# Performance work log

Hardware: AMD Instinct MI355X
Metric: run time of the kernel (lower is better)

## Reference

```python
import jax, jax.numpy as jnp
import numpy as np

B, T, D_IN, D_H, N_H = 8, 1024, 512, 64, 8
PAD_TAIL = 128


def setup_inputs() -> dict:
    key = jax.random.key(0)
    ks = jax.random.split(key, 7)
    keys = jax.random.normal(ks[0], (B, T, D_IN), jnp.float32)
    queries = jax.random.normal(ks[1], (B, T, D_IN), jnp.float32)
    values = jax.random.normal(ks[2], (B, T, D_IN), jnp.float32)
    # truncated_normal(stddev=0.01) in the original; plain normal*0.01 is a faithful stand-in
    Wk = jax.random.normal(ks[3], (D_IN, D_H, N_H), jnp.float32) * 0.01
    Wq = jax.random.normal(ks[4], (D_IN, D_H, N_H), jnp.float32) * 0.01
    Wv = jax.random.normal(ks[5], (D_IN, D_H, N_H), jnp.float32) * 0.01
    key_seq = jax.random.randint(ks[6], (B, T), 0, 32000)
    key_seq = key_seq.at[:, -PAD_TAIL:].set(-1)  # -1 marks padding positions
    return {"keys": keys, "queries": queries, "values": values,
            "Wk": Wk, "Wq": Wq, "Wv": Wv, "key_seq": key_seq}


def reference(keys, queries, values, Wk, Wq, Wv, key_seq):
    # projections: (b, t, i) x (i, d, h) -> (b, t, d, h)
    Kh = jnp.einsum('bti,idh->btdh', keys, Wk)
    Qh = jnp.einsum('bti,idh->btdh', queries, Wq)
    Vh = jnp.einsum('bti,idh->btdh', values, Wv)

    # scores: i indexes keys, j indexes queries -> (b, Tk, Tq, h)
    scores = jnp.einsum('bidh,bjdh->bijh', Kh, Qh)

    dt = scores.dtype
    # padding mask over key positions (key_seq == -1 -> -1000)
    pad_mask = (-1000.0 * (1.0 - jnp.sign(key_seq + 1).astype(dt)))[:, :, None, None]
    # causal mask: disallow key index i > query index j (matrix_band_part(_, 0, -1) keeps i<=j)
    Tk, Tq = Kh.shape[1], Qh.shape[1]
    caus_mask = -1000.0 * jnp.tril(jnp.ones((Tk, Tq), dt), k=-1)
    mask = pad_mask + caus_mask[None, :, :, None]

    # NB: original adds mask BEFORE scaling, so the -1000 is also scaled. Keep that order.
    hidden_size = Kh.shape[2]
    scores = (scores + mask) / (hidden_size ** 0.5)

    # softmax over the key axis (axis=1)
    attn = jax.nn.softmax(scores, axis=1)

    # aggregate values: (b, i, j, h) x (b, i, d, h) -> (b, j, d, h)
    h_t = jnp.einsum('bijh,bidh->bjdh', attn, Vh)

    # tf.concat(tf.split(h_t, H, axis=-1), axis=2)[:, :, :, 0]
    # == per-head feature blocks laid out head-major along the feature axis
    b, j, d, nh = h_t.shape
    return h_t.transpose(0, 1, 3, 2).reshape(b, j, nh * d)
```

## Files before the change

kernel.cpp:

```cpp
#include <hip/hip_runtime.h>
#include <hip/hip_bf16.h>

#define B_SZ 8
#define T_SZ 1024
#define D_IN 512
#define D_H  64
#define N_H  8

typedef __hip_bfloat16 bf16;
using short8  = __attribute__((ext_vector_type(8))) short;
using short4v = __attribute__((ext_vector_type(4))) short;
using f32x4   = __attribute__((ext_vector_type(4))) float;

__device__ __forceinline__ unsigned short f2bf(float f) {
    union { __hip_bfloat16 b; unsigned short u; } c;
    c.b = __float2bfloat16(f);
    return c.u;
}

__device__ __forceinline__ void glds16(const unsigned short* g, unsigned short* l) {
    __builtin_amdgcn_global_load_lds(
        (const __attribute__((address_space(1))) unsigned int*)g,
        (__attribute__((address_space(3))) unsigned int*)l, 16, 0, 0);
}

__global__ __launch_bounds__(256) void wt_kernel(
    const float* __restrict__ Wk, const float* __restrict__ Wq,
    const float* __restrict__ Wv, unsigned short* __restrict__ Wt)
{
    const int mat = blockIdx.y;
    const float* W = (mat == 0) ? Wk : (mat == 1) ? Wq : Wv;
    int idx = blockIdx.x * 256 + threadIdx.x;
    float v = W[idx];
    int k = idx >> 9, c = idx & 511;
    int h = c & 7, d = c >> 3;
    int ks = (k & ~63) | ((k & 63) ^ ((d & 7) << 3));
    Wt[(((size_t)mat * 8 + h) * 64 + d) * 512 + ks] = f2bf(v);
}

__global__ __launch_bounds__(256, 3) void proj_kernel(
    const float* __restrict__ keys, const float* __restrict__ queries,
    const float* __restrict__ values,
    const unsigned short* __restrict__ Wt, unsigned short* __restrict__ KQVb)
{
    const int tid = threadIdx.x;
    const int m0  = blockIdx.x * 128;
    const int n0  = blockIdx.y * 128;
    const int mat = blockIdx.z;

    const float* X = (mat == 0) ? keys : (mat == 1) ? queries : values;
    const unsigned short* WT = Wt + (size_t)mat * (512 * 512);
    unsigned short* P = KQVb + (size_t)mat * ((size_t)B_SZ * N_H * T_SZ * D_H);

    __shared__ __align__(16) unsigned short Xst[128 * 64];
    __shared__ __align__(16) unsigned short Wst[2][128 * 64];

    const int wid = tid >> 6, lane = tid & 63;
    const int quad = lane >> 4, l15 = lane & 15;
    const int wr = (wid >> 1) * 64, wc = (wid & 1) * 64;

    const int ur = tid >> 3, uch = tid & 7;
    const int wrow  = wid * 32 + (lane >> 3);
    const int wcol8 = (lane & 7) * 8;

    f32x4 acc[4][4];
    #pragma unroll
    for (int i = 0; i < 4; ++i)
        #pragma unroll
        for (int n = 0; n < 4; ++n) acc[i][n] = (f32x4){0.f, 0.f, 0.f, 0.f};

    const float4* X4 = (const float4*)X;

    #pragma unroll
    for (int q = 0; q < 4; ++q)
        glds16(&WT[(size_t)(n0 + wrow + q * 8) * 512 + wcol8],
               &Wst[0][(wid * 4 + q) * 512]);
    float4 xr[4][2];
    #pragma unroll
    for (int q = 0; q < 4; ++q) {
        int r = ur + q * 32;
        xr[q][0] = X4[(size_t)(m0 + r) * 128 + uch * 2];
        xr[q][1] = X4[(size_t)(m0 + r) * 128 + uch * 2 + 1];
    }

    int wb = 0;
    for (int kc = 0; kc < 8; ++kc) {
        #pragma unroll
        for (int q = 0; q < 4; ++q) {
            int r = ur + q * 32;
            float4 a = xr[q][0], b = xr[q][1];
            short8 s8 = {(short)f2bf(a.x), (short)f2bf(a.y),
                         (short)f2bf(a.z), (short)f2bf(a.w),
                         (short)f2bf(b.x), (short)f2bf(b.y),
                         (short)f2bf(b.z), (short)f2bf(b.w)};
            *(short8*)&Xst[r * 64 + ((uch * 8) ^ ((r & 7) << 3))] = s8;
        }
        if (kc < 7) {
            const int k0n = (kc + 1) * 64;
            #pragma unroll
            for (int q = 0; q < 4; ++q)
                glds16(&WT[(size_t)(n0 + wrow + q * 8) * 512 + k0n + wcol8],
                       &Wst[wb ^ 1][(wid * 4 + q) * 512]);
            #pragma unroll
            for (int q = 0; q < 4; ++q) {
                int r = ur + q * 32;
                xr[q][0] = X4[(size_t)(m0 + r) * 128 + (k0n >> 2) + uch * 2];
                xr[q][1] = X4[(size_t)(m0 + r) * 128 + (k0n >> 2) + uch * 2 + 1];
            }
        }
        asm volatile("s_waitcnt lgkmcnt(0)" ::: "memory");
        __builtin_amdgcn_s_barrier();

        #pragma unroll
        for (int ic = 0; ic < 2; ++ic) {
            const int sc = ic * 32 + quad * 8;
            short8 af[4], bfr[4];
            #pragma unroll
            for (int mt = 0; mt < 4; ++mt) {
                int r = wr + mt * 16 + l15;
                af[mt] = *(const short8*)&Xst[r * 64 + (sc ^ ((r & 7) << 3))];
            }
            #pragma unroll
            for (int nt = 0; nt < 4; ++nt) {
                int r = wc + nt * 16 + l15;
                bfr[nt] = *(const short8*)&Wst[wb][r * 64 + (sc ^ ((r & 7) << 3))];
            }
            #pragma unroll
            for (int mt = 0; mt < 4; ++mt)
                #pragma unroll
                for (int nt = 0; nt < 4; ++nt)
                    acc[mt][nt] = __builtin_amdgcn_mfma_f32_16x16x32_bf16(
                        af[mt], bfr[nt], acc[mt][nt], 0, 0, 0);
        }

        asm volatile("s_waitcnt lgkmcnt(0)" ::: "memory");
        __builtin_amdgcn_s_barrier();
        wb ^= 1;
    }

    #pragma unroll
    for (int mt = 0; mt < 4; ++mt)
        #pragma unroll
        for (int r = 0; r < 4; ++r) {
            int mrow = m0 + wr + mt * 16 + quad * 4 + r;
            int bb = mrow >> 10, t = mrow & 1023;
            #pragma unroll
            for (int nt = 0; nt < 4; ++nt) {
                int c = n0 + wc + nt * 16 + l15;
                int h = c >> 6, d = c & 63;
                P[(((size_t)(bb * N_H + h)) * T_SZ + t) * D_H + d] =
                    f2bf(acc[mt][nt][r]);
            }
        }
}

#define SCALE  0.18033688f
#define MASKV -180.33688f

__global__ __launch_bounds__(512, 4) void attn_kernel(
    const unsigned short* __restrict__ Qb, const unsigned short* __restrict__ Kb,
    const unsigned short* __restrict__ Vb,
    const int* __restrict__ key_seq, float* __restrict__ out)
{
    const int tid  = threadIdx.x;
    const int bid  = blockIdx.x;
    const int pair = bid >> 6;
    const int b    = (bid >> 3) & 7;
    const int h    = bid & 7;
    const int wid  = tid >> 6, lane = tid & 63;
    const int quad = lane >> 4, l15 = lane & 15;

    __shared__ __align__(16) unsigned short Kst[2][64 * 72];
    __shared__ __align__(16) unsigned short VTst[2][64 * 72];
    __shared__ __align__(16) float spadf[2][64];
    __shared__ int tflags[16];

    const size_t bh = (size_t)(b * N_H + h) * T_SZ;

    const int strip_j0 = (wid < 4) ? (15 - pair) * 64 : pair * 64;
    const int j0w = strip_j0 + (wid & 3) * 16;
    const int jg  = j0w + l15;
    const int ntmax = 16 - pair;

    short8 qf0 = *(const short8*)&Qb[(bh + jg) * D_H + quad * 8];
    short8 qf1 = *(const short8*)&Qb[(bh + jg) * D_H + 32 + quad * 8];

    {
        int ka  = key_seq[b * T_SZ + wid * 64 + lane];
        int kb2 = key_seq[b * T_SZ + 512 + wid * 64 + lane];
        unsigned long long ba  = __ballot(ka  != -1);
        unsigned long long bb2 = __ballot(kb2 != -1);
        if (lane == 0) {
            tflags[wid]     = (ba  != 0ull ? 1 : 0) | (ba  != ~0ull ? 2 : 0);
            tflags[8 + wid] = (bb2 != 0ull ? 1 : 0) | (bb2 != ~0ull ? 2 : 0);
        }
    }

    const int sk_row = tid >> 3, sk_c = tid & 7;
    const int sv_i = lane, sv_ch = wid;
    const int sv_col = (sv_i & 3) | ((sv_i & 16) >> 2) | ((sv_i & 4) << 1)
                     | ((sv_i & 8) << 1) | (sv_i & 32);

    short8 kreg = *(const short8*)&Kb[(bh + sk_row) * D_H + sk_c * 8];
    short8 vreg = *(const short8*)&Vb[(bh + sv_i) * D_H + sv_ch * 8];
    int ksv = (tid < 64) ? key_seq[b * T_SZ + tid] : -1;

    __syncthreads();

    unsigned tmask = 1u, pmask = 0u;
    #pragma unroll
    for (int t = 0; t < 16; ++t) {
        int f = tflags[t];
        tmask |= (unsigned)(f & 1) << t;
        pmask |= (unsigned)((f >> 1) & 1) << t;
    }
    tmask &= (unsigned)((1ull << ntmax) - 1ull);
    tmask |= 1u;

    *(short8*)&Kst[0][sk_row * 72 + sk_c * 8] = kreg;
    #pragma unroll
    for (int e = 0; e < 8; ++e)
        VTst[0][(sv_ch * 8 + e) * 72 + sv_col] = (unsigned short)vreg[e];
    if (tid < 64) spadf[0][tid] = (ksv == -1) ? MASKV : 0.f;
    __syncthreads();

    float m = -1e30f, l = 0.f;
    f32x4 o0 = {0.f,0.f,0.f,0.f}, o1 = o0, o2 = o0, o3 = o0;

    unsigned rem = tmask & ~1u;
    int tcur = 0, nb = 0;
    for (;;) {
        int tnext = -1;
        if (rem) { tnext = __ffs((int)rem) - 1; rem &= rem - 1; }
        if (tnext >= 0) {
            const size_t r0 = bh + tnext * 64;
            kreg = *(const short8*)&Kb[(r0 + sk_row) * D_H + sk_c * 8];
            vreg = *(const short8*)&Vb[(r0 + sv_i) * D_H + sv_ch * 8];
            if (tid < 64) ksv = key_seq[b * T_SZ + tnext * 64 + tid];
        }

        const int i0 = tcur * 64;
        if (i0 <= j0w + 15) {
            const bool haspad = (pmask >> tcur) & 1u;
            const bool needC  = (i0 + 63 > j0w);
            float sv[16];
            #pragma unroll
            for (int it = 0; it < 4; ++it) {
                f32x4 s = {0.f,0.f,0.f,0.f};
                short8 a0 = *(const short8*)&Kst[nb][(it*16 + l15) * 72 + quad*8];
                s = __builtin_amdgcn_mfma_f32_16x16x32_bf16(a0, qf0, s, 0, 0, 0);
                short8 a1 = *(const short8*)&Kst[nb][(it*16 + l15) * 72 + 32 + quad*8];
                s = __builtin_amdgcn_mfma_f32_16x16x32_bf16(a1, qf1, s, 0, 0, 0);
                f32x4 sp = {0.f,0.f,0.f,0.f};
                if (haspad) sp = *(const f32x4*)&spadf[nb][it*16 + quad*4];
                #pragma unroll
                for (int r = 0; r < 4; ++r) {
                    float v = __builtin_fmaf(s[r], SCALE, sp[r]);
                    if (needC && (i0 + it*16 + quad*4 + r > jg)) v += MASKV;
                    sv[it*4 + r] = v;
                }
            }

            float mt = sv[0];
            #pragma unroll
            for (int k = 1; k < 16; ++k) mt = fmaxf(mt, sv[k]);
            mt = fmaxf(mt, __shfl_xor(mt, 16));
            mt = fmaxf(mt, __shfl_xor(mt, 32));
            const float mnew  = fmaxf(m, mt);
            const float alpha = exp2f(m - mnew);
            float p[16], ls = 0.f;
            #pragma unroll
            for (int k = 0; k < 16; ++k) {
                p[k] = exp2f(sv[k] - mnew);
                ls += p[k];
            }
            ls += __shfl_xor(ls, 16);
            ls += __shfl_xor(ls, 32);
            l = l * alpha + ls;
            m = mnew;
            o0 *= alpha; o1 *= alpha; o2 *= alpha; o3 *= alpha;

            short8 pf0, pf1;
            #pragma unroll
            for (int e = 0; e < 8; ++e) {
                pf0[e] = (short)f2bf(p[e]);
                pf1[e] = (short)f2bf(p[8 + e]);
            }
            short8 a;
            a = *(const short8*)&VTst[nb][(     l15) * 72 +      quad * 8];
            o0 = __builtin_amdgcn_mfma_f32_16x16x32_bf16(a, pf0, o0, 0, 0, 0);
            a = *(const short8*)&VTst[nb][(     l15) * 72 + 32 + quad * 8];
            o0 = __builtin_amdgcn_mfma_f32_16x16x32_bf16(a, pf1, o0, 0, 0, 0);
            a = *(const short8*)&VTst[nb][(16 + l15) * 72 +      quad * 8];
            o1 = __builtin_amdgcn_mfma_f32_16x16x32_bf16(a, pf0, o1, 0, 0, 0);
            a = *(const short8*)&VTst[nb][(16 + l15) * 72 + 32 + quad * 8];
            o1 = __builtin_amdgcn_mfma_f32_16x16x32_bf16(a, pf1, o1, 0, 0, 0);
            a = *(const short8*)&VTst[nb][(32 + l15) * 72 +      quad * 8];
            o2 = __builtin_amdgcn_mfma_f32_16x16x32_bf16(a, pf0, o2, 0, 0, 0);
            a = *(const short8*)&VTst[nb][(32 + l15) * 72 + 32 + quad * 8];
            o2 = __builtin_amdgcn_mfma_f32_16x16x32_bf16(a, pf1, o2, 0, 0, 0);
            a = *(const short8*)&VTst[nb][(48 + l15) * 72 +      quad * 8];
            o3 = __builtin_amdgcn_mfma_f32_16x16x32_bf16(a, pf0, o3, 0, 0, 0);
            a = *(const short8*)&VTst[nb][(48 + l15) * 72 + 32 + quad * 8];
            o3 = __builtin_amdgcn_mfma_f32_16x16x32_bf16(a, pf1, o3, 0, 0, 0);
        }

        if (tnext < 0) break;

        const int nb2 = nb ^ 1;
        *(short8*)&Kst[nb2][sk_row * 72 + sk_c * 8] = kreg;
        #pragma unroll
        for (int e = 0; e < 8; ++e)
            VTst[nb2][(sv_ch * 8 + e) * 72 + sv_col] = (unsigned short)vreg[e];
        if (tid < 64) spadf[nb2][tid] = (ksv == -1) ? MASKV : 0.f;
        __syncthreads();
        tcur = tnext; nb = nb2;
    }

    const float inv = 1.f / l;
    float* op = out + ((size_t)b * T_SZ + jg) * (N_H * D_H) + h * D_H + quad * 4;
    *(f32x4*)(op +  0) = o0 * inv;
    *(f32x4*)(op + 16) = o1 * inv;
    *(f32x4*)(op + 32) = o2 * inv;
    *(f32x4*)(op + 48) = o3 * inv;
}

extern "C" void kernel_launch(void* const* d_in, const int* in_sizes, int n_in,
                              void* d_out, int out_size, void* d_ws, size_t ws_size,
                              hipStream_t stream) {
    const float* keys    = (const float*)d_in[0];
    const float* queries = (const float*)d_in[1];
    const float* values  = (const float*)d_in[2];
    const float* Wk      = (const float*)d_in[3];
    const float* Wq      = (const float*)d_in[4];
    const float* Wv      = (const float*)d_in[5];
    const int*   key_seq = (const int*)d_in[6];

    const size_t per = (size_t)B_SZ * N_H * T_SZ * D_H;
    unsigned short* KQVb = (unsigned short*)d_ws;
    unsigned short* Kb = KQVb;
    unsigned short* Qb = KQVb + per;
    unsigned short* Vb = KQVb + 2 * per;
    unsigned short* Wt = KQVb + 3 * per;

    wt_kernel<<<dim3(512 * 512 / 256, 3), 256, 0, stream>>>(Wk, Wq, Wv, Wt);
    proj_kernel<<<dim3(64, 4, 3), 256, 0, stream>>>(
        keys, queries, values, Wt, KQVb);
    attn_kernel<<<dim3(512), dim3(512), 0, stream>>>(
        Qb, Kb, Vb, key_seq, (float*)d_out);
}
```

Before: 153.2 us.

## Pre-convert activations to bf16 in a merged prep kernel, load A fragments directly

```diff
diff --git a/kernel.cpp b/kernel.cpp
--- a/kernel.cpp
+++ b/kernel.cpp
@@ -24,106 +24,106 @@
         (__attribute__((address_space(3))) unsigned int*)l, 16, 0, 0);
 }
 
-__global__ __launch_bounds__(256) void wt_kernel(
-    const float* __restrict__ Wk, const float* __restrict__ Wq,
-    const float* __restrict__ Wv, unsigned short* __restrict__ Wt)
-{
-    const int mat = blockIdx.y;
-    const float* W = (mat == 0) ? Wk : (mat == 1) ? Wq : Wv;
-    int idx = blockIdx.x * 256 + threadIdx.x;
-    float v = W[idx];
-    int k = idx >> 9, c = idx & 511;
-    int h = c & 7, d = c >> 3;
-    int ks = (k & ~63) | ((k & 63) ^ ((d & 7) << 3));
-    Wt[(((size_t)mat * 8 + h) * 64 + d) * 512 + ks] = f2bf(v);
-}
-
-__global__ __launch_bounds__(256, 3) void proj_kernel(
+__global__ __launch_bounds__(256) void prep_kernel(
     const float* __restrict__ keys, const float* __restrict__ queries,
     const float* __restrict__ values,
+    const float* __restrict__ Wk, const float* __restrict__ Wq,
+    const float* __restrict__ Wv,
+    unsigned short* __restrict__ Wt, unsigned short* __restrict__ Xb)
+{
+    const int bid = blockIdx.x;
+    const int tid = threadIdx.x;
+    if (bid < 768) {
+        const int mat = bid >> 8;
+        const float* W = (mat == 0) ? Wk : (mat == 1) ? Wq : Wv;
+        unsigned short* WTo = Wt + (size_t)mat * (512 * 512);
+        const int base = (bid & 255) * 1024;
+        #pragma unroll
+        for (int q = 0; q < 4; ++q) {
+            int idx = base + tid + q * 256;
+            float v = W[idx];
+            int k = idx >> 9, c = idx & 511;
+            int h = c & 7, d = c >> 3;
+            int ks = (k & ~63) | ((k & 63) ^ ((d & 7) << 3));
+            WTo[((size_t)h * 64 + d) * 512 + ks] = f2bf(v);
+        }
+    } else {
+        const int j = bid - 768;
+        const int mat = j >> 11;
+        const float* X = (mat == 0) ? keys : (mat == 1) ? queries : values;
+        unsigned short* XO = Xb + ((size_t)mat << 22);
+        const int e0 = ((j & 2047) << 11) + tid * 8;
+        float4 a = *(const float4*)&X[e0];
+        float4 b = *(const float4*)&X[e0 + 4];
+        short8 s8 = {(short)f2bf(a.x), (short)f2bf(a.y),
+                     (short)f2bf(a.z), (short)f2bf(a.w),
+                     (short)f2bf(b.x), (short)f2bf(b.y),
+                     (short)f2bf(b.z), (short)f2bf(b.w)};
+        *(short8*)&XO[e0] = s8;
+    }
+}
+
+__global__ __launch_bounds__(256, 3) void proj_kernel(
+    const unsigned short* __restrict__ Xb,
     const unsigned short* __restrict__ Wt, unsigned short* __restrict__ KQVb)
 {
     const int tid = threadIdx.x;
-    const int m0  = blockIdx.x * 128;
-    const int n0  = blockIdx.y * 128;
-    const int mat = blockIdx.z;
-
-    const float* X = (mat == 0) ? keys : (mat == 1) ? queries : values;
+    const int bid = blockIdx.x;
+    const int xcd = bid & 7, ii = bid >> 3;
+    const int n0  = (ii & 3) * 128;
+    const int key = (ii >> 2) + xcd * 24;
+    const int mat = key >> 6;
+    const int m0  = (key & 63) * 128;
+
+    const unsigned short* X  = Xb + ((size_t)mat << 22);
     const unsigned short* WT = Wt + (size_t)mat * (512 * 512);
     unsigned short* P = KQVb + (size_t)mat * ((size_t)B_SZ * N_H * T_SZ * D_H);
 
-    __shared__ __align__(16) unsigned short Xst[128 * 64];
     __shared__ __align__(16) unsigned short Wst[2][128 * 64];
 
     const int wid = tid >> 6, lane = tid & 63;
     const int quad = lane >> 4, l15 = lane & 15;
     const int wr = (wid >> 1) * 64, wc = (wid & 1) * 64;
 
-    const int ur = tid >> 3, uch = tid & 7;
     const int wrow  = wid * 32 + (lane >> 3);
     const int wcol8 = (lane & 7) * 8;
+    const int arow = m0 + wr + l15;
 
     f32x4 acc[4][4];
     #pragma unroll
     for (int i = 0; i < 4; ++i)
         #pragma unroll
         for (int n = 0; n < 4; ++n) acc[i][n] = (f32x4){0.f, 0.f, 0.f, 0.f};
-
-    const float4* X4 = (const float4*)X;
 
     #pragma unroll
     for (int q = 0; q < 4; ++q)
         glds16(&WT[(size_t)(n0 + wrow + q * 8) * 512 + wcol8],
                &Wst[0][(wid * 4 + q) * 512]);
-    float4 xr[4][2];
-    #pragma unroll
-    for (int q = 0; q < 4; ++q) {
-        int r = ur + q * 32;
-        xr[q][0] = X4[(size_t)(m0 + r) * 128 + uch * 2];
-        xr[q][1] = X4[(size_t)(m0 + r) * 128 + uch * 2 + 1];
-    }
-
-    int wb = 0;
+    asm volatile("s_waitcnt vmcnt(0)" ::: "memory");
+    __builtin_amdgcn_s_barrier();
+
+    int pbuf = 0;
     for (int kc = 0; kc < 8; ++kc) {
-        #pragma unroll
-        for (int q = 0; q < 4; ++q) {
-            int r = ur + q * 32;
-            float4 a = xr[q][0], b = xr[q][1];
-            short8 s8 = {(short)f2bf(a.x), (short)f2bf(a.y),
-                         (short)f2bf(a.z), (short)f2bf(a.w),
-                         (short)f2bf(b.x), (short)f2bf(b.y),
-                         (short)f2bf(b.z), (short)f2bf(b.w)};
-            *(short8*)&Xst[r * 64 + ((uch * 8) ^ ((r & 7) << 3))] = s8;
-        }
+        const int k0 = kc * 64;
         if (kc < 7) {
-            const int k0n = (kc + 1) * 64;
+            const int k0n = k0 + 64;
             #pragma unroll
             for (int q = 0; q < 4; ++q)
                 glds16(&WT[(size_t)(n0 + wrow + q * 8) * 512 + k0n + wcol8],
-                       &Wst[wb ^ 1][(wid * 4 + q) * 512]);
-            #pragma unroll
-            for (int q = 0; q < 4; ++q) {
-                int r = ur + q * 32;
-                xr[q][0] = X4[(size_t)(m0 + r) * 128 + (k0n >> 2) + uch * 2];
-                xr[q][1] = X4[(size_t)(m0 + r) * 128 + (k0n >> 2) + uch * 2 + 1];
-            }
-        }
-        asm volatile("s_waitcnt lgkmcnt(0)" ::: "memory");
-        __builtin_amdgcn_s_barrier();
-
+                       &Wst[pbuf ^ 1][(wid * 4 + q) * 512]);
+        }
+        __builtin_amdgcn_sched_barrier(0);
         #pragma unroll
         for (int ic = 0; ic < 2; ++ic) {
             const int sc = ic * 32 + quad * 8;
             short8 af[4], bfr[4];
             #pragma unroll
-            for (int mt = 0; mt < 4; ++mt) {
-                int r = wr + mt * 16 + l15;
-                af[mt] = *(const short8*)&Xst[r * 64 + (sc ^ ((r & 7) << 3))];
-            }
+            for (int mt = 0; mt < 4; ++mt)
+                af[mt] = *(const short8*)&X[(size_t)(arow + mt * 16) * 512 + k0 + sc];
             #pragma unroll
             for (int nt = 0; nt < 4; ++nt) {
                 int r = wc + nt * 16 + l15;
-                bfr[nt] = *(const short8*)&Wst[wb][r * 64 + (sc ^ ((r & 7) << 3))];
+                bfr[nt] = *(const short8*)&Wst[pbuf][r * 64 + (sc ^ ((r & 7) << 3))];
             }
             #pragma unroll
             for (int mt = 0; mt < 4; ++mt)
@@ -132,10 +132,9 @@
                     acc[mt][nt] = __builtin_amdgcn_mfma_f32_16x16x32_bf16(
                         af[mt], bfr[nt], acc[mt][nt], 0, 0, 0);
         }
-
         asm volatile("s_waitcnt lgkmcnt(0)" ::: "memory");
         __builtin_amdgcn_s_barrier();
-        wb ^= 1;
+        pbuf ^= 1;
     }
 
     #pragma unroll
@@ -342,10 +341,11 @@
     unsigned short* Qb = KQVb + per;
     unsigned short* Vb = KQVb + 2 * per;
     unsigned short* Wt = KQVb + 3 * per;
-
-    wt_kernel<<<dim3(512 * 512 / 256, 3), 256, 0, stream>>>(Wk, Wq, Wv, Wt);
-    proj_kernel<<<dim3(64, 4, 3), 256, 0, stream>>>(
-        keys, queries, values, Wt, KQVb);
+    unsigned short* Xb = Wt + (size_t)3 * 512 * 512;
+
+    prep_kernel<<<dim3(768 + 6144), 256, 0, stream>>>(
+        keys, queries, values, Wk, Wq, Wv, Wt, Xb);
+    proj_kernel<<<dim3(768), 256, 0, stream>>>(Xb, Wt, KQVb);
     attn_kernel<<<dim3(512), dim3(512), 0, stream>>>(
         Qb, Kb, Vb, key_seq, (float*)d_out);
 }
```

New measurement: 164.1 us. 7.1% more time.

## Load projection activations directly from global and triple-buffer weight tiles

Applied to the files above, without the earlier changes.

```diff
diff --git a/kernel.cpp b/kernel.cpp
--- a/kernel.cpp
+++ b/kernel.cpp
@@ -52,16 +52,15 @@
     const unsigned short* WT = Wt + (size_t)mat * (512 * 512);
     unsigned short* P = KQVb + (size_t)mat * ((size_t)B_SZ * N_H * T_SZ * D_H);
 
-    __shared__ __align__(16) unsigned short Xst[128 * 64];
-    __shared__ __align__(16) unsigned short Wst[2][128 * 64];
+    __shared__ __align__(16) unsigned short Wst[3][128 * 64];
 
     const int wid = tid >> 6, lane = tid & 63;
     const int quad = lane >> 4, l15 = lane & 15;
     const int wr = (wid >> 1) * 64, wc = (wid & 1) * 64;
 
-    const int ur = tid >> 3, uch = tid & 7;
     const int wrow  = wid * 32 + (lane >> 3);
     const int wcol8 = (lane & 7) * 8;
+    const int arow = m0 + wr + l15;
 
     f32x4 acc[4][4];
     #pragma unroll
@@ -69,61 +68,49 @@
         #pragma unroll
         for (int n = 0; n < 4; ++n) acc[i][n] = (f32x4){0.f, 0.f, 0.f, 0.f};
 
-    const float4* X4 = (const float4*)X;
-
     #pragma unroll
     for (int q = 0; q < 4; ++q)
         glds16(&WT[(size_t)(n0 + wrow + q * 8) * 512 + wcol8],
                &Wst[0][(wid * 4 + q) * 512]);
-    float4 xr[4][2];
-    #pragma unroll
-    for (int q = 0; q < 4; ++q) {
-        int r = ur + q * 32;
-        xr[q][0] = X4[(size_t)(m0 + r) * 128 + uch * 2];
-        xr[q][1] = X4[(size_t)(m0 + r) * 128 + uch * 2 + 1];
-    }
-
-    int wb = 0;
+    #pragma unroll
+    for (int q = 0; q < 4; ++q)
+        glds16(&WT[(size_t)(n0 + wrow + q * 8) * 512 + 64 + wcol8],
+               &Wst[1][(wid * 4 + q) * 512]);
+
     for (int kc = 0; kc < 8; ++kc) {
-        #pragma unroll
-        for (int q = 0; q < 4; ++q) {
-            int r = ur + q * 32;
-            float4 a = xr[q][0], b = xr[q][1];
-            short8 s8 = {(short)f2bf(a.x), (short)f2bf(a.y),
-                         (short)f2bf(a.z), (short)f2bf(a.w),
-                         (short)f2bf(b.x), (short)f2bf(b.y),
-                         (short)f2bf(b.z), (short)f2bf(b.w)};
-            *(short8*)&Xst[r * 64 + ((uch * 8) ^ ((r & 7) << 3))] = s8;
-        }
-        if (kc < 7) {
-            const int k0n = (kc + 1) * 64;
+        const int k0 = kc * 64;
+        if (kc < 7) asm volatile("s_waitcnt vmcnt(4)" ::: "memory");
+        else        asm volatile("s_waitcnt vmcnt(0)" ::: "memory");
+        __builtin_amdgcn_s_barrier();
+        if (kc < 6) {
+            const int k2 = k0 + 128;
             #pragma unroll
             for (int q = 0; q < 4; ++q)
-                glds16(&WT[(size_t)(n0 + wrow + q * 8) * 512 + k0n + wcol8],
-                       &Wst[wb ^ 1][(wid * 4 + q) * 512]);
-            #pragma unroll
-            for (int q = 0; q < 4; ++q) {
-                int r = ur + q * 32;
-                xr[q][0] = X4[(size_t)(m0 + r) * 128 + (k0n >> 2) + uch * 2];
-                xr[q][1] = X4[(size_t)(m0 + r) * 128 + (k0n >> 2) + uch * 2 + 1];
-            }
-        }
-        asm volatile("s_waitcnt lgkmcnt(0)" ::: "memory");
-        __builtin_amdgcn_s_barrier();
-
+                glds16(&WT[(size_t)(n0 + wrow + q * 8) * 512 + k2 + wcol8],
+                       &Wst[(kc + 2) % 3][(wid * 4 + q) * 512]);
+        }
+        __builtin_amdgcn_sched_barrier(0);
+
+        const unsigned short* Wb = Wst[kc % 3];
         #pragma unroll
         for (int ic = 0; ic < 2; ++ic) {
             const int sc = ic * 32 + quad * 8;
-            short8 af[4], bfr[4];
+            short8 af[4];
             #pragma unroll
             for (int mt = 0; mt < 4; ++mt) {
-                int r = wr + mt * 16 + l15;
-                af[mt] = *(const short8*)&Xst[r * 64 + (sc ^ ((r & 7) << 3))];
-            }
+                const float* ap = &X[(size_t)(arow + mt * 16) * 512 + k0 + sc];
+                float4 a = *(const float4*)ap;
+                float4 b = *(const float4*)(ap + 4);
+                af[mt] = (short8){(short)f2bf(a.x), (short)f2bf(a.y),
+                                  (short)f2bf(a.z), (short)f2bf(a.w),
+                                  (short)f2bf(b.x), (short)f2bf(b.y),
+                                  (short)f2bf(b.z), (short)f2bf(b.w)};
+            }
+            short8 bfr[4];
             #pragma unroll
             for (int nt = 0; nt < 4; ++nt) {
                 int r = wc + nt * 16 + l15;
-                bfr[nt] = *(const short8*)&Wst[wb][r * 64 + (sc ^ ((r & 7) << 3))];
+                bfr[nt] = *(const short8*)&Wb[r * 64 + (sc ^ ((r & 7) << 3))];
             }
             #pragma unroll
             for (int mt = 0; mt < 4; ++mt)
@@ -132,10 +119,6 @@
                     acc[mt][nt] = __builtin_amdgcn_mfma_f32_16x16x32_bf16(
                         af[mt], bfr[nt], acc[mt][nt], 0, 0, 0);
         }
-
-        asm volatile("s_waitcnt lgkmcnt(0)" ::: "memory");
-        __builtin_amdgcn_s_barrier();
-        wb ^= 1;
     }
 
     #pragma unroll
```

After: 177.5 us. 15.8% more time.
